# Kernel tuning notes

Hardware: AMD Instinct MI355X
Metric: run time of the kernel (lower is better)

Reference implementation:

```python
import math
import jax, jax.numpy as jnp
import numpy as np

C = 8.0  # decay constant from __init__
_MIN_RAD, _MAX_RAD = 0.9, 0.999


def block_diag_linear(x, w):
    # x: (B,T,D), w: (H, bs, bs) with D = H*bs
    B, T, D = x.shape
    H, bs, _ = w.shape
    xh = x.reshape(B, T, H, bs)
    return jnp.einsum('bthd,hde->bthe', xh, w).reshape(B, T, D)


def linear_scan(a, b):
    # h_t = a_t * h_{t-1} + b_t, h_{-1}=0, via associative scan:
    # (a1,b1) o (a2,b2) = (a1*a2, a2*b1 + b2)
    def op(l, r):
        a1, b1 = l
        a2, b2 = r
        return (a1 * a2, a2 * b1 + b2)
    return jax.lax.associative_scan(op, (a, b), axis=1)[1]


def setup_inputs() -> dict:
    key = jax.random.key(0)
    k1, k2, k3, k4 = jax.random.split(key, 4)
    B, T, D, H = 4, 4096, 1024, 8
    bs = D // H
    x = jax.random.normal(k1, (B, T, D), dtype=jnp.float32)
    std = 1.0 / math.sqrt(bs)
    w_in = jax.random.normal(k2, (H, bs, bs), dtype=jnp.float32) * std
    w_a = jax.random.normal(k3, (H, bs, bs), dtype=jnp.float32) * std
    # a_param init: softplus^{-1} of uniform in [-log(max_rad)/c, -log(min_rad)/c]
    sp = jax.random.uniform(k4, (D,), dtype=jnp.float32,
                            minval=-math.log(_MAX_RAD) / C,
                            maxval=-math.log(_MIN_RAD) / C)
    a_param = jnp.log(jnp.exp(sp) - 1.0 + 1e-8)
    return {"x": x, "a_param": a_param, "w_in": w_in, "w_a": w_a}


def reference(x, a_param, w_in, w_a):
    # RG-LRU forward with h_prev = None
    gate_x = jax.nn.sigmoid(block_diag_linear(x, w_in))  # input gate i_t
    gate_a = jax.nn.sigmoid(block_diag_linear(x, w_a))   # recurrence gate r_t
    log_a = -C * jax.nn.softplus(a_param) * gate_a       # (B,T,D)
    a = jnp.exp(log_a)
    multiplier = jnp.sqrt(1.0 - jnp.exp(2.0 * log_a))    # sqrt(1 - a^2)
    b = multiplier * (gate_x * x)
    y = linear_scan(a, b)                                 # (B,T,D)
    h_last = y[:, -1, :]
    return y, h_last
```

## Files before the change

kernel.cpp:

```cpp
#include <hip/hip_runtime.h>

#define B_ 4
#define T_ 4096
#define D_ 1024
#define H_ 8
#define M_ (B_*T_)

typedef unsigned short u16;
typedef unsigned int u32;
typedef __attribute__((ext_vector_type(8))) short s16x8;
typedef __attribute__((ext_vector_type(4))) float f32x4;

#define LOG2E 1.4426950408889634f

__device__ __forceinline__ float ex2(float x){
#if __has_builtin(__builtin_amdgcn_exp2f)
  return __builtin_amdgcn_exp2f(x);
#else
  return exp2f(x);
#endif
}
__device__ __forceinline__ float rcpf(float x){
#if __has_builtin(__builtin_amdgcn_rcpf)
  return __builtin_amdgcn_rcpf(x);
#else
  return __fdividef(1.0f, x);
#endif
}
__device__ __forceinline__ float bf2f(u16 u){
  union { u32 i; float f; } v; v.i = ((u32)u) << 16; return v.f;
}
__device__ __forceinline__ u16 f2bf(float f){
  union { float f; u32 i; } v; v.f = f;
  u32 i = v.i;
  return (u16)((i + 0x7FFFu + ((i >> 16) & 1u)) >> 16);
}
__device__ __forceinline__ float sigf(float z){
  return rcpf(1.0f + ex2(-LOG2E * z));
}
__device__ __forceinline__ s16x8 cvt8(float4 a, float4 b){
  s16x8 r;
  r[0] = (short)(__float_as_uint(a.x) >> 16);
  r[1] = (short)(__float_as_uint(a.y) >> 16);
  r[2] = (short)(__float_as_uint(a.z) >> 16);
  r[3] = (short)(__float_as_uint(a.w) >> 16);
  r[4] = (short)(__float_as_uint(b.x) >> 16);
  r[5] = (short)(__float_as_uint(b.y) >> 16);
  r[6] = (short)(__float_as_uint(b.z) >> 16);
  r[7] = (short)(__float_as_uint(b.w) >> 16);
  return r;
}

__global__ __launch_bounds__(256) void k0_transpose(const float* __restrict__ w_in,
                                                    const float* __restrict__ w_a,
                                                    u16* __restrict__ wt){
  __shared__ float ls[128][132];
  const int blk = blockIdx.x;
  const float* src = (blk < 8 ? w_in : w_a) + (size_t)(blk & 7) * 128 * 128;
  u16* dst = wt + (size_t)blk * 128 * 128;
  const int tid = threadIdx.x;
  const int r0 = tid >> 5;
  const int c0 = (tid & 31) * 4;
  #pragma unroll
  for (int it = 0; it < 16; ++it){
    int r = r0 + it * 8;
    *(float4*)(&ls[r][c0]) = *(const float4*)(src + r * 128 + c0);
  }
  __syncthreads();
  #pragma unroll
  for (int it = 0; it < 16; ++it){
    int e = r0 + it * 8;
    ushort4 u;
    u.x = f2bf(ls[c0 + 0][e]);
    u.y = f2bf(ls[c0 + 1][e]);
    u.z = f2bf(ls[c0 + 2][e]);
    u.w = f2bf(ls[c0 + 3][e]);
    *(ushort4*)(dst + e * 128 + c0) = u;
  }
}

__global__ __launch_bounds__(256, 3) void k1_gemm_scan(
    const float* __restrict__ x, const float* __restrict__ a_param,
    const u16* __restrict__ wt, u32* __restrict__ pack,
    float* __restrict__ Ablk, float* __restrict__ Yblk)
{
  __shared__ __align__(16) union SMem {
    u16 w[2][64][136];
    u32 p[128 * 68];
  } SU;
  __shared__ float waveC[4][64][2];
  __shared__ float aspS[64];

  const int blk = blockIdx.x;
  const int hh  = blk & 15;
  const int h = hh >> 1, eh = hh & 1;
  const int mbg = blk >> 4;
  const int batch = mbg >> 5;
  const int tb    = mbg & 31;
  const int mbase = mbg * 128;
  const int tid = threadIdx.x;
  const int wv = tid >> 6, lane = tid & 63;
  const int q = lane >> 4, l = lane & 15;

  {
    uint4 wbuf[8];
    #pragma unroll
    for (int it = 0; it < 8; ++it){
      int idx = tid + it * 256;
      int row = idx >> 4;
      int mat = row >> 6, e = row & 63;
      int c8 = (idx & 15) * 8;
      wbuf[it] = *(const uint4*)(wt + (size_t)mat * (8 * 128 * 128)
                                  + (h * 128 + eh * 64 + e) * 128 + c8);
    }
    #pragma unroll
    for (int it = 0; it < 8; ++it){
      int idx = tid + it * 256;
      int row = idx >> 4;
      int c8 = (idx & 15) * 8;
      *(uint4*)(&SU.w[0][0][0] + row * 136 + c8) = wbuf[it];
    }
  }

  const float* xr0 = x + (size_t)(mbase + wv * 32 + l) * D_ + h * 128;
  const float* xr1 = xr0 + 16 * D_;
  float4 A0[4][2], A1[4][2];
  #pragma unroll
  for (int kb = 0; kb < 4; ++kb){
    int ko = kb * 32 + q * 8;
    A0[kb][0] = *(const float4*)(xr0 + ko);
    A0[kb][1] = *(const float4*)(xr0 + ko + 4);
    A1[kb][0] = *(const float4*)(xr1 + ko);
    A1[kb][1] = *(const float4*)(xr1 + ko + 4);
  }
  if (tid < 64)
    aspS[tid] = 8.0f * log1pf(__expf(a_param[h * 128 + eh * 64 + tid]));
  __syncthreads();

  f32x4 accX[2][4], accG[2][4];
  #pragma unroll
  for (int mt = 0; mt < 2; ++mt)
    #pragma unroll
    for (int nt = 0; nt < 4; ++nt){ accX[mt][nt] = (f32x4)0.0f; accG[mt][nt] = (f32x4)0.0f; }

  #pragma unroll
  for (int kb = 0; kb < 4; ++kb){
    const int ko = kb * 32 + q * 8;
    s16x8 a0 = cvt8(A0[kb][0], A0[kb][1]);
    s16x8 a1 = cvt8(A1[kb][0], A1[kb][1]);
    #pragma unroll
    for (int nt = 0; nt < 4; ++nt){
      s16x8 bi = *(const s16x8*)(&SU.w[0][nt * 16 + l][ko]);
      s16x8 ba = *(const s16x8*)(&SU.w[1][nt * 16 + l][ko]);
      accX[0][nt] = __builtin_amdgcn_mfma_f32_16x16x32_bf16(a0, bi, accX[0][nt], 0, 0, 0);
      accX[1][nt] = __builtin_amdgcn_mfma_f32_16x16x32_bf16(a1, bi, accX[1][nt], 0, 0, 0);
      accG[0][nt] = __builtin_amdgcn_mfma_f32_16x16x32_bf16(a0, ba, accG[0][nt], 0, 0, 0);
      accG[1][nt] = __builtin_amdgcn_mfma_f32_16x16x32_bf16(a1, ba, accG[1][nt], 0, 0, 0);
    }
  }

  float av[2][4][4], bv[2][4][4];
  #pragma unroll
  for (int mt = 0; mt < 2; ++mt){
    #pragma unroll
    for (int nt = 0; nt < 4; ++nt){
      const int el = nt * 16 + l;
      const int col = eh * 64 + el;
      const float asp = aspS[el];
      #pragma unroll
      for (int r = 0; r < 4; ++r){
        const int row = wv * 32 + mt * 16 + q * 4 + r;
        float gx = sigf(accX[mt][nt][r]);
        float ga = sigf(accG[mt][nt][r]);
        float la = -asp * ga;
        float a  = ex2(LOG2E * la);
        float mult = sqrtf(fmaxf(1.0f - a * a, 0.0f));
        float xv = x[(size_t)(mbase + row) * D_ + h * 128 + col];
        av[mt][nt][r] = a;
        bv[mt][nt][r] = mult * gx * xv;
      }
    }
  }

  float preA[2][4], preY[2][4];
  #pragma unroll
  for (int nt = 0; nt < 4; ++nt){
    const int col = nt * 16 + l;
    float S0A = 1.0f, S0Y = 0.0f;
    #pragma unroll
    for (int mt = 0; mt < 2; ++mt){
      float a0 = av[mt][nt][0], a1 = av[mt][nt][1], a2 = av[mt][nt][2], a3 = av[mt][nt][3];
      float b0 = bv[mt][nt][0], b1 = bv[mt][nt][1], b2 = bv[mt][nt][2], b3 = bv[mt][nt][3];
      float TA = (a0 * a1) * (a2 * a3);
      float TY = fmaf(a3, fmaf(a2, fmaf(a1, b0, b1), b2), b3);
      float QA0 = __shfl(TA, l,      64), QY0 = __shfl(TY, l,      64);
      float QA1 = __shfl(TA, l + 16, 64), QY1 = __shfl(TY, l + 16, 64);
      float QA2 = __shfl(TA, l + 32, 64), QY2 = __shfl(TY, l + 32, 64);
      float QA3 = __shfl(TA, l + 48, 64), QY3 = __shfl(TY, l + 48, 64);
      float P1A = QA0,       P1Y = QY0;
      float P2A = P1A * QA1, P2Y = fmaf(QA1, P1Y, QY1);
      float P3A = P2A * QA2, P3Y = fmaf(QA2, P2Y, QY2);
      float QpA = (q == 0) ? 1.0f : ((q == 1) ? P1A : ((q == 2) ? P2A : P3A));
      float QpY = (q == 0) ? 0.0f : ((q == 1) ? P1Y : ((q == 2) ? P2Y : P3Y));
      float S16A = P3A * QA3, S16Y = fmaf(QA3, P3Y, QY3);
      float MA = (mt == 0) ? 1.0f : S0A;
      float MY = (mt == 0) ? 0.0f : S0Y;
      preA[mt][nt] = MA * QpA;
      preY[mt][nt] = fmaf(QpA, MY, QpY);
      if (mt == 0){ S0A = S16A; S0Y = S16Y; }
      else {
        float WA = S0A * S16A, WY = fmaf(S16A, S0Y, S16Y);
        if (lane < 16){ waveC[wv][col][0] = WA; waveC[wv][col][1] = WY; }
      }
    }
  }
  __syncthreads();

  float wpA[4], wpY[4];
  #pragma unroll
  for (int nt = 0; nt < 4; ++nt){
    int col = nt * 16 + l;
    float A = 1.0f, Y = 0.0f;
    #pragma unroll
    for (int w2 = 0; w2 < 3; ++w2){
      if (w2 < wv){
        float cA = waveC[w2][col][0], cY = waveC[w2][col][1];
        Y = fmaf(cA, Y, cY);
        A = A * cA;
      }
    }
    wpA[nt] = A; wpY[nt] = Y;
  }

  if (wv == 0){
    const int col = lane;
    float bA = waveC[0][col][0], bY = waveC[0][col][1];
    float cA1 = waveC[1][col][0], cY1 = waveC[1][col][1];
    float cA2 = waveC[2][col][0], cY2 = waveC[2][col][1];
    float cA3 = waveC[3][col][0], cY3 = waveC[3][col][1];
    bY = fmaf(cA1, bY, cY1); bA *= cA1;
    bY = fmaf(cA2, bY, cY2); bA *= cA2;
    bY = fmaf(cA3, bY, cY3); bA *= cA3;
    int gi = (batch * 32 + tb) * D_ + h * 128 + eh * 64 + col;
    Ablk[gi] = bA;
    Yblk[gi] = bY;
  }

  #pragma unroll
  for (int nt = 0; nt < 4; ++nt){
    const int col = nt * 16 + l;
    float basev = wpY[nt];
    #pragma unroll
    for (int mt = 0; mt < 2; ++mt){
      float v  = fmaf(preA[mt][nt], basev, preY[mt][nt]);
      float cA = wpA[nt] * preA[mt][nt];
      const int R0 = wv * 32 + mt * 16 + q * 4;
      #pragma unroll
      for (int r = 0; r < 4; ++r){
        v  = fmaf(av[mt][nt][r], v, bv[mt][nt][r]);
        cA = cA * av[mt][nt][r];
        SU.p[(R0 + r) * 68 + col] = (u32)f2bf(v) | ((u32)f2bf(cA) << 16);
      }
    }
  }
  __syncthreads();

  {
    u32* pg = pack + (size_t)mbase * D_ + h * 128 + eh * 64;
    #pragma unroll
    for (int it = 0; it < 8; ++it){
      int idx = tid + it * 256;
      int row = idx >> 4;
      int c4 = (idx & 15) * 4;
      uint4 v = *(uint4*)(&SU.p[row * 68 + c4]);
      *(uint4*)(pg + (size_t)row * D_ + c4) = v;
    }
  }
}

__global__ __launch_bounds__(256) void k3_fixup(const u32* pack,
                                               const float* __restrict__ Ablk,
                                               const float* __restrict__ Yblk,
                                               float* y_out, float* hlast){
  const int cg = blockIdx.x;
  const int r0 = cg * 16;
  const int batch = r0 >> 12;
  const int tb = (r0 & (T_ - 1)) >> 7;
  const int d0 = threadIdx.x * 4;

  float4 hv; hv.x = 0.0f; hv.y = 0.0f; hv.z = 0.0f; hv.w = 0.0f;
  for (int t = 0; t < tb; ++t){
    int gi = (batch * 32 + t) * D_ + d0;
    float4 A = *(const float4*)(&Ablk[gi]);
    float4 Y = *(const float4*)(&Yblk[gi]);
    hv.x = fmaf(A.x, hv.x, Y.x);
    hv.y = fmaf(A.y, hv.y, Y.y);
    hv.z = fmaf(A.z, hv.z, Y.z);
    hv.w = fmaf(A.w, hv.w, Y.w);
  }

  float4 yv;
  #pragma unroll
  for (int t = 0; t < 16; ++t){
    int idx = (r0 + t) * D_ + d0;
    uint4 w = *(const uint4*)(&pack[idx]);
    yv.x = fmaf(bf2f((u16)(w.x >> 16)), hv.x, bf2f((u16)(w.x & 0xFFFFu)));
    yv.y = fmaf(bf2f((u16)(w.y >> 16)), hv.y, bf2f((u16)(w.y & 0xFFFFu)));
    yv.z = fmaf(bf2f((u16)(w.z >> 16)), hv.z, bf2f((u16)(w.z & 0xFFFFu)));
    yv.w = fmaf(bf2f((u16)(w.w >> 16)), hv.w, bf2f((u16)(w.w & 0xFFFFu)));
    *(float4*)(&y_out[idx]) = yv;
  }

  if (((r0 + 16) & (T_ - 1)) == 0){
    *(float4*)(&hlast[batch * D_ + d0]) = yv;
  }
}

extern "C" void kernel_launch(void* const* d_in, const int* in_sizes, int n_in,
                              void* d_out, int out_size, void* d_ws, size_t ws_size,
                              hipStream_t stream) {
  const float* x    = (const float*)d_in[0];
  const float* ap   = (const float*)d_in[1];
  const float* w_in = (const float*)d_in[2];
  const float* w_a  = (const float*)d_in[3];
  float* y = (float*)d_out;
  float* hlast = y + (size_t)B_ * T_ * D_;
  u32* pack = (u32*)d_out;

  char* ws = (char*)d_ws;
  u16*   wt   = (u16*)(ws);
  float* Ablk = (float*)(ws + 524288);
  float* Yblk = (float*)(ws + 1048576);

  k0_transpose<<<16, 256, 0, stream>>>(w_in, w_a, wt);
  k1_gemm_scan<<<128 * 16, 256, 0, stream>>>(x, ap, wt, pack, Ablk, Yblk);
  k3_fixup<<<1024, 256, 0, stream>>>(pack, Ablk, Yblk, y, hlast);
}
```

Before: 174.4 us.

## Fuse chunk fixup into GEMM-scan kernel via decoupled look-back carry chain

Replaces the separate fixup kernel with a single-pass chained scan. Each block takes a dynamic tile index from an atomic counter, waits on a flag for the previous time-chunk's inclusive aggregate, publishes its own aggregate, and writes the final fp32 y directly. This drops the bf16 pack round-trip through global memory and the second kernel's read and write of the full output. The cost is serialized waiting along the 32 time chunks per channel group, plus a small kernel that zeroes the flags. The output also gains precision because the bf16 packing step is gone.

```diff
diff --git a/kernel.cpp b/kernel.cpp
--- a/kernel.cpp
+++ b/kernel.cpp
@@ -26,9 +26,6 @@
 #else
   return __fdividef(1.0f, x);
 #endif
-}
-__device__ __forceinline__ float bf2f(u16 u){
-  union { u32 i; float f; } v; v.i = ((u32)u) << 16; return v.f;
 }
 __device__ __forceinline__ u16 f2bf(float f){
   union { float f; u32 i; } v; v.f = f;
@@ -51,6 +48,11 @@
   return r;
 }
 
+__global__ __launch_bounds__(256) void kz_zero(u32* __restrict__ flags){
+  int i = blockIdx.x * 256 + threadIdx.x;
+  if (i < 2049) flags[i] = 0u;
+}
+
 __global__ __launch_bounds__(256) void k0_transpose(const float* __restrict__ w_in,
                                                     const float* __restrict__ w_a,
                                                     u16* __restrict__ wt){
@@ -79,26 +81,32 @@
   }
 }
 
-__global__ __launch_bounds__(256, 3) void k1_gemm_scan(
+__global__ __launch_bounds__(256, 3) void k1_fused(
     const float* __restrict__ x, const float* __restrict__ a_param,
-    const u16* __restrict__ wt, u32* __restrict__ pack,
-    float* __restrict__ Ablk, float* __restrict__ Yblk)
+    const u16* __restrict__ wt, float* __restrict__ y_out,
+    float* __restrict__ hlast, float* __restrict__ Aagg,
+    float* __restrict__ Yagg, u32* __restrict__ flags)
 {
   __shared__ __align__(16) union SMem {
     u16 w[2][64][136];
-    u32 p[128 * 68];
+    float yf[128 * 68];
   } SU;
   __shared__ float waveC[4][64][2];
   __shared__ float aspS[64];
-
-  const int blk = blockIdx.x;
-  const int hh  = blk & 15;
+  __shared__ float hinS[64];
+  __shared__ u32 vbS;
+
+  const int tid = threadIdx.x;
+  if (tid == 0) vbS = atomicAdd(&flags[2048], 1u);
+  __syncthreads();
+  const u32 vb = vbS;
+  const int tb = vb >> 6;
+  const int c  = vb & 63;
+  const int batch = c >> 4;
+  const int hh = c & 15;
   const int h = hh >> 1, eh = hh & 1;
-  const int mbg = blk >> 4;
-  const int batch = mbg >> 5;
-  const int tb    = mbg & 31;
+  const int mbg = batch * 32 + tb;
   const int mbase = mbg * 128;
-  const int tid = threadIdx.x;
   const int wv = tid >> 6, lane = tid & 63;
   const int q = lane >> 4, l = lane & 15;
 
@@ -241,78 +249,60 @@
     bY = fmaf(cA1, bY, cY1); bA *= cA1;
     bY = fmaf(cA2, bY, cY2); bA *= cA2;
     bY = fmaf(cA3, bY, cY3); bA *= cA3;
-    int gi = (batch * 32 + tb) * D_ + h * 128 + eh * 64 + col;
-    Ablk[gi] = bA;
-    Yblk[gi] = bY;
-  }
+
+    float EA = 1.0f, EY = 0.0f;
+    if (tb > 0){
+      const int pe = c * 32 + (tb - 1);
+      u32 st;
+      do {
+        st = __hip_atomic_load(&flags[pe], __ATOMIC_ACQUIRE, __HIP_MEMORY_SCOPE_AGENT);
+        if (st == 0u) __builtin_amdgcn_s_sleep(1);
+      } while (st == 0u);
+      EA = __hip_atomic_load(&Aagg[pe * 64 + col], __ATOMIC_RELAXED, __HIP_MEMORY_SCOPE_AGENT);
+      EY = __hip_atomic_load(&Yagg[pe * 64 + col], __ATOMIC_RELAXED, __HIP_MEMORY_SCOPE_AGENT);
+    }
+    const float IA = bA * EA;
+    const float IY = fmaf(bA, EY, bY);
+    const int me = c * 32 + tb;
+    __hip_atomic_store(&Aagg[me * 64 + col], IA, __ATOMIC_RELAXED, __HIP_MEMORY_SCOPE_AGENT);
+    __hip_atomic_store(&Yagg[me * 64 + col], IY, __ATOMIC_RELAXED, __HIP_MEMORY_SCOPE_AGENT);
+    __threadfence();
+    if (lane == 0)
+      __hip_atomic_store(&flags[me], 2u, __ATOMIC_RELEASE, __HIP_MEMORY_SCOPE_AGENT);
+    hinS[col] = EY;
+    if (tb == 31)
+      hlast[batch * D_ + h * 128 + eh * 64 + col] = IY;
+  }
+  __syncthreads();
 
   #pragma unroll
   for (int nt = 0; nt < 4; ++nt){
     const int col = nt * 16 + l;
-    float basev = wpY[nt];
+    const float hin = hinS[col];
     #pragma unroll
     for (int mt = 0; mt < 2; ++mt){
-      float v  = fmaf(preA[mt][nt], basev, preY[mt][nt]);
-      float cA = wpA[nt] * preA[mt][nt];
+      float v = fmaf(preA[mt][nt], wpY[nt], preY[mt][nt]);
+      v = fmaf(wpA[nt] * preA[mt][nt], hin, v);
       const int R0 = wv * 32 + mt * 16 + q * 4;
       #pragma unroll
       for (int r = 0; r < 4; ++r){
-        v  = fmaf(av[mt][nt][r], v, bv[mt][nt][r]);
-        cA = cA * av[mt][nt][r];
-        SU.p[(R0 + r) * 68 + col] = (u32)f2bf(v) | ((u32)f2bf(cA) << 16);
+        v = fmaf(av[mt][nt][r], v, bv[mt][nt][r]);
+        SU.yf[(R0 + r) * 68 + col] = v;
       }
     }
   }
   __syncthreads();
 
   {
-    u32* pg = pack + (size_t)mbase * D_ + h * 128 + eh * 64;
+    float* pg = y_out + (size_t)mbase * D_ + h * 128 + eh * 64;
     #pragma unroll
     for (int it = 0; it < 8; ++it){
       int idx = tid + it * 256;
       int row = idx >> 4;
       int c4 = (idx & 15) * 4;
-      uint4 v = *(uint4*)(&SU.p[row * 68 + c4]);
-      *(uint4*)(pg + (size_t)row * D_ + c4) = v;
-    }
-  }
-}
-
-__global__ __launch_bounds__(256) void k3_fixup(const u32* pack,
-                                               const float* __restrict__ Ablk,
-                                               const float* __restrict__ Yblk,
-                                               float* y_out, float* hlast){
-  const int cg = blockIdx.x;
-  const int r0 = cg * 16;
-  const int batch = r0 >> 12;
-  const int tb = (r0 & (T_ - 1)) >> 7;
-  const int d0 = threadIdx.x * 4;
-
-  float4 hv; hv.x = 0.0f; hv.y = 0.0f; hv.z = 0.0f; hv.w = 0.0f;
-  for (int t = 0; t < tb; ++t){
-    int gi = (batch * 32 + t) * D_ + d0;
-    float4 A = *(const float4*)(&Ablk[gi]);
-    float4 Y = *(const float4*)(&Yblk[gi]);
-    hv.x = fmaf(A.x, hv.x, Y.x);
-    hv.y = fmaf(A.y, hv.y, Y.y);
-    hv.z = fmaf(A.z, hv.z, Y.z);
-    hv.w = fmaf(A.w, hv.w, Y.w);
-  }
-
-  float4 yv;
-  #pragma unroll
-  for (int t = 0; t < 16; ++t){
-    int idx = (r0 + t) * D_ + d0;
-    uint4 w = *(const uint4*)(&pack[idx]);
-    yv.x = fmaf(bf2f((u16)(w.x >> 16)), hv.x, bf2f((u16)(w.x & 0xFFFFu)));
-    yv.y = fmaf(bf2f((u16)(w.y >> 16)), hv.y, bf2f((u16)(w.y & 0xFFFFu)));
-    yv.z = fmaf(bf2f((u16)(w.z >> 16)), hv.z, bf2f((u16)(w.z & 0xFFFFu)));
-    yv.w = fmaf(bf2f((u16)(w.w >> 16)), hv.w, bf2f((u16)(w.w & 0xFFFFu)));
-    *(float4*)(&y_out[idx]) = yv;
-  }
-
-  if (((r0 + 16) & (T_ - 1)) == 0){
-    *(float4*)(&hlast[batch * D_ + d0]) = yv;
+      float4 v = *(float4*)(&SU.yf[row * 68 + c4]);
+      *(float4*)(pg + (size_t)row * D_ + c4) = v;
+    }
   }
 }
 
@@ -325,14 +315,14 @@
   const float* w_a  = (const float*)d_in[3];
   float* y = (float*)d_out;
   float* hlast = y + (size_t)B_ * T_ * D_;
-  u32* pack = (u32*)d_out;
 
   char* ws = (char*)d_ws;
   u16*   wt   = (u16*)(ws);
-  float* Ablk = (float*)(ws + 524288);
-  float* Yblk = (float*)(ws + 1048576);
-
+  float* Aagg = (float*)(ws + 524288);
+  float* Yagg = (float*)(ws + 1048576);
+  u32*   flags= (u32*)(ws + 1572864);
+
+  kz_zero<<<9, 256, 0, stream>>>(flags);
   k0_transpose<<<16, 256, 0, stream>>>(w_in, w_a, wt);
-  k1_gemm_scan<<<128 * 16, 256, 0, stream>>>(x, ap, wt, pack, Ablk, Yblk);
-  k3_fixup<<<1024, 256, 0, stream>>>(pack, Ablk, Yblk, y, hlast);
-}
+  k1_fused<<<2048, 256, 0, stream>>>(x, ap, wt, y, hlast, Aagg, Yagg, flags);
+}
```

Measured after the change: 665.2 us. +281.4%, slower.

## Merge column halves into one 512-thread block per head and row tile

Applied to the files above, without the earlier changes.

Each k1 block now covers all 128 output columns of a head with 8 waves (4 row slabs by 2 column halves), where before two 256-thread blocks each handled 64 columns. Both halves now share one block's x tile loads and weight staging, and the extra block-index bookkeeping goes away, halving the grid size. In exchange each block needs more LDS (about 70KB for the weight and pack union), which may limit how many blocks fit per CU, and each block is larger.

```diff
diff --git a/kernel.cpp b/kernel.cpp
--- a/kernel.cpp
+++ b/kernel.cpp
@@ -79,50 +79,52 @@
   }
 }
 
-__global__ __launch_bounds__(256, 3) void k1_gemm_scan(
+__global__ __launch_bounds__(512, 4) void k1_gemm_scan(
     const float* __restrict__ x, const float* __restrict__ a_param,
     const u16* __restrict__ wt, u32* __restrict__ pack,
     float* __restrict__ Ablk, float* __restrict__ Yblk)
 {
   __shared__ __align__(16) union SMem {
-    u16 w[2][64][136];
-    u32 p[128 * 68];
+    u16 w[2][128][136];
+    u32 p[128 * 132];
   } SU;
-  __shared__ float waveC[4][64][2];
-  __shared__ float aspS[64];
+  __shared__ float waveC[4][128][2];
+  __shared__ float aspS[128];
 
   const int blk = blockIdx.x;
-  const int hh  = blk & 15;
-  const int h = hh >> 1, eh = hh & 1;
-  const int mbg = blk >> 4;
+  const int h   = blk & 7;
+  const int mbg = blk >> 3;
   const int batch = mbg >> 5;
   const int tb    = mbg & 31;
   const int mbase = mbg * 128;
   const int tid = threadIdx.x;
-  const int wv = tid >> 6, lane = tid & 63;
+  const int wv2 = tid >> 6;
+  const int rs = wv2 & 3;
+  const int ch = wv2 >> 2;
+  const int lane = tid & 63;
   const int q = lane >> 4, l = lane & 15;
 
   {
     uint4 wbuf[8];
     #pragma unroll
     for (int it = 0; it < 8; ++it){
-      int idx = tid + it * 256;
+      int idx = tid + it * 512;
       int row = idx >> 4;
-      int mat = row >> 6, e = row & 63;
+      int mat = row >> 7, e = row & 127;
       int c8 = (idx & 15) * 8;
       wbuf[it] = *(const uint4*)(wt + (size_t)mat * (8 * 128 * 128)
-                                  + (h * 128 + eh * 64 + e) * 128 + c8);
+                                  + (h * 128 + e) * 128 + c8);
     }
     #pragma unroll
     for (int it = 0; it < 8; ++it){
-      int idx = tid + it * 256;
+      int idx = tid + it * 512;
       int row = idx >> 4;
       int c8 = (idx & 15) * 8;
       *(uint4*)(&SU.w[0][0][0] + row * 136 + c8) = wbuf[it];
     }
   }
 
-  const float* xr0 = x + (size_t)(mbase + wv * 32 + l) * D_ + h * 128;
+  const float* xr0 = x + (size_t)(mbase + rs * 32 + l) * D_ + h * 128;
   const float* xr1 = xr0 + 16 * D_;
   float4 A0[4][2], A1[4][2];
   #pragma unroll
@@ -133,8 +135,8 @@
     A1[kb][0] = *(const float4*)(xr1 + ko);
     A1[kb][1] = *(const float4*)(xr1 + ko + 4);
   }
-  if (tid < 64)
-    aspS[tid] = 8.0f * log1pf(__expf(a_param[h * 128 + eh * 64 + tid]));
+  if (tid < 128)
+    aspS[tid] = 8.0f * log1pf(__expf(a_param[h * 128 + tid]));
   __syncthreads();
 
   f32x4 accX[2][4], accG[2][4];
@@ -150,8 +152,9 @@
     s16x8 a1 = cvt8(A1[kb][0], A1[kb][1]);
     #pragma unroll
     for (int nt = 0; nt < 4; ++nt){
-      s16x8 bi = *(const s16x8*)(&SU.w[0][nt * 16 + l][ko]);
-      s16x8 ba = *(const s16x8*)(&SU.w[1][nt * 16 + l][ko]);
+      const int e = ch * 64 + nt * 16 + l;
+      s16x8 bi = *(const s16x8*)(&SU.w[0][e][ko]);
+      s16x8 ba = *(const s16x8*)(&SU.w[1][e][ko]);
       accX[0][nt] = __builtin_amdgcn_mfma_f32_16x16x32_bf16(a0, bi, accX[0][nt], 0, 0, 0);
       accX[1][nt] = __builtin_amdgcn_mfma_f32_16x16x32_bf16(a1, bi, accX[1][nt], 0, 0, 0);
       accG[0][nt] = __builtin_amdgcn_mfma_f32_16x16x32_bf16(a0, ba, accG[0][nt], 0, 0, 0);
@@ -164,12 +167,11 @@
   for (int mt = 0; mt < 2; ++mt){
     #pragma unroll
     for (int nt = 0; nt < 4; ++nt){
-      const int el = nt * 16 + l;
-      const int col = eh * 64 + el;
-      const float asp = aspS[el];
+      const int col = ch * 64 + nt * 16 + l;
+      const float asp = aspS[col];
       #pragma unroll
       for (int r = 0; r < 4; ++r){
-        const int row = wv * 32 + mt * 16 + q * 4 + r;
+        const int row = rs * 32 + mt * 16 + q * 4 + r;
         float gx = sigf(accX[mt][nt][r]);
         float ga = sigf(accG[mt][nt][r]);
         float la = -asp * ga;
@@ -185,7 +187,7 @@
   float preA[2][4], preY[2][4];
   #pragma unroll
   for (int nt = 0; nt < 4; ++nt){
-    const int col = nt * 16 + l;
+    const int col = ch * 64 + nt * 16 + l;
     float S0A = 1.0f, S0Y = 0.0f;
     #pragma unroll
     for (int mt = 0; mt < 2; ++mt){
@@ -210,7 +212,7 @@
       if (mt == 0){ S0A = S16A; S0Y = S16Y; }
       else {
         float WA = S0A * S16A, WY = fmaf(S16A, S0Y, S16Y);
-        if (lane < 16){ waveC[wv][col][0] = WA; waveC[wv][col][1] = WY; }
+        if (lane < 16){ waveC[rs][col][0] = WA; waveC[rs][col][1] = WY; }
       }
     }
   }
@@ -219,11 +221,11 @@
   float wpA[4], wpY[4];
   #pragma unroll
   for (int nt = 0; nt < 4; ++nt){
-    int col = nt * 16 + l;
+    int col = ch * 64 + nt * 16 + l;
     float A = 1.0f, Y = 0.0f;
     #pragma unroll
     for (int w2 = 0; w2 < 3; ++w2){
-      if (w2 < wv){
+      if (w2 < rs){
         float cA = waveC[w2][col][0], cY = waveC[w2][col][1];
         Y = fmaf(cA, Y, cY);
         A = A * cA;
@@ -232,8 +234,8 @@
     wpA[nt] = A; wpY[nt] = Y;
   }
 
-  if (wv == 0){
-    const int col = lane;
+  if (rs == 0){
+    const int col = ch * 64 + lane;
     float bA = waveC[0][col][0], bY = waveC[0][col][1];
     float cA1 = waveC[1][col][0], cY1 = waveC[1][col][1];
     float cA2 = waveC[2][col][0], cY2 = waveC[2][col][1];
@@ -241,38 +243,38 @@
     bY = fmaf(cA1, bY, cY1); bA *= cA1;
     bY = fmaf(cA2, bY, cY2); bA *= cA2;
     bY = fmaf(cA3, bY, cY3); bA *= cA3;
-    int gi = (batch * 32 + tb) * D_ + h * 128 + eh * 64 + col;
+    int gi = (batch * 32 + tb) * D_ + h * 128 + col;
     Ablk[gi] = bA;
     Yblk[gi] = bY;
   }
 
   #pragma unroll
   for (int nt = 0; nt < 4; ++nt){
-    const int col = nt * 16 + l;
+    const int col = ch * 64 + nt * 16 + l;
     float basev = wpY[nt];
     #pragma unroll
     for (int mt = 0; mt < 2; ++mt){
       float v  = fmaf(preA[mt][nt], basev, preY[mt][nt]);
       float cA = wpA[nt] * preA[mt][nt];
-      const int R0 = wv * 32 + mt * 16 + q * 4;
+      const int R0 = rs * 32 + mt * 16 + q * 4;
       #pragma unroll
       for (int r = 0; r < 4; ++r){
         v  = fmaf(av[mt][nt][r], v, bv[mt][nt][r]);
         cA = cA * av[mt][nt][r];
-        SU.p[(R0 + r) * 68 + col] = (u32)f2bf(v) | ((u32)f2bf(cA) << 16);
+        SU.p[(R0 + r) * 132 + col] = (u32)f2bf(v) | ((u32)f2bf(cA) << 16);
       }
     }
   }
   __syncthreads();
 
   {
-    u32* pg = pack + (size_t)mbase * D_ + h * 128 + eh * 64;
+    u32* pg = pack + (size_t)mbase * D_ + h * 128;
     #pragma unroll
     for (int it = 0; it < 8; ++it){
-      int idx = tid + it * 256;
-      int row = idx >> 4;
-      int c4 = (idx & 15) * 4;
-      uint4 v = *(uint4*)(&SU.p[row * 68 + c4]);
+      int idx = tid + it * 512;
+      int row = idx >> 5;
+      int c4 = (idx & 31) * 4;
+      uint4 v = *(uint4*)(&SU.p[row * 132 + c4]);
       *(uint4*)(pg + (size_t)row * D_ + c4) = v;
     }
   }
@@ -333,6 +335,6 @@
   float* Yblk = (float*)(ws + 1048576);
 
   k0_transpose<<<16, 256, 0, stream>>>(w_in, w_a, wt);
-  k1_gemm_scan<<<128 * 16, 256, 0, stream>>>(x, ap, wt, pack, Ablk, Yblk);
+  k1_gemm_scan<<<1024, 512, 0, stream>>>(x, ap, wt, pack, Ablk, Yblk);
   k3_fixup<<<1024, 256, 0, stream>>>(pack, Ablk, Yblk, y, hlast);
 }
```

Result: slower. 199.4 us (+14.3%).
